# Optimization experiments

Measured on AMD Instinct MI355X. Metric: run time of the kernel, lower is better.

The kernel has to match this reference:

```python
import jax, jax.numpy as jnp
import numpy as np

T, D, H, E, K = 8192, 2048, 7168, 8, 2


def setup_inputs() -> dict:
    key = jax.random.key(0)
    ks = jax.random.split(key, 5)
    s = 0.02
    return {
        "x": jax.random.normal(ks[0], (T, D), jnp.float32),
        "gate_w": jax.random.normal(ks[1], (E, D), jnp.float32) * s,
        "w1": jax.random.normal(ks[2], (E, H, D), jnp.float32) * s,
        "w2": jax.random.normal(ks[3], (E, H, D), jnp.float32) * s,
        "w3": jax.random.normal(ks[4], (E, H, D), jnp.float32) * s,
    }


def reference(x, gate_w, w1, w2, w3):
    # gate logits [T, E]
    logits = x @ gate_w.T
    vals, idx = jax.lax.top_k(logits, K)                      # [T, K]
    w = jax.nn.softmax(vals.astype(jnp.float32), axis=-1).astype(x.dtype)
    # per-token routing weight for each expert (0 if not selected) [T, E]
    tok = jnp.arange(x.shape[0])
    expert_w = jnp.zeros((x.shape[0], E), x.dtype).at[tok[:, None], idx].add(w)

    # scan over experts: dense SwiGLU per expert, weighted accumulate
    def body(acc, ws):
        w1e, w2e, w3e, we = ws  # [H,D],[H,D],[H,D],[T]
        y = (jax.nn.silu(x @ w1e.T) * (x @ w3e.T)) @ w2e      # [T, D]
        return acc + we[:, None] * y, None

    res, _ = jax.lax.scan(body, jnp.zeros_like(x), (w1, w2, w3, expert_w.T))
    return res
```

## Files before the change

### kernel.cpp

```cpp
#include <hip/hip_runtime.h>

#define TT   8192
#define DDIM 2048
#define HDIM 7168
#define NEXP 8
#define MT   32
#define NT1  (HDIM / 128)
#define NT2  (DDIM / 256)
#define KSPL 2
#define NTILE_MAX 72

typedef __attribute__((ext_vector_type(8))) short bf16x8;
typedef __attribute__((ext_vector_type(8))) short short8v;
typedef __attribute__((ext_vector_type(4))) short short4v;
typedef __attribute__((ext_vector_type(4))) float f32x4;

__device__ __forceinline__ unsigned short f2bf(float f) {
  unsigned int u = __builtin_bit_cast(unsigned int, f);
  u += 0x7fffu + ((u >> 16) & 1u);
  return (unsigned short)(u >> 16);
}

__device__ __forceinline__ float bf2f(unsigned short h) {
  unsigned int u = ((unsigned int)h) << 16;
  return __builtin_bit_cast(float, u);
}

__device__ __forceinline__ void gload_lds16(const void* gp, void* lp) {
  __builtin_amdgcn_global_load_lds((__attribute__((address_space(1))) void*)gp,
                                   (__attribute__((address_space(3))) void*)lp,
                                   16, 0, 0);
}

__device__ __forceinline__ void mfma16(f32x4& c, bf16x8 a, bf16x8 b) {
  c = __builtin_amdgcn_mfma_f32_16x16x32_bf16(a, b, c, 0, 0, 0);
}

__device__ __forceinline__ void wg_barrier() {
  asm volatile("" ::: "memory");
  __builtin_amdgcn_s_barrier();
  asm volatile("" ::: "memory");
}

#define PH(H, BA, BB, RDB, STG, SRCP, SOFF, VM)                              \
  do {                                                                       \
    if (RDB) {                                                               \
      _Pragma("unroll")                                                      \
      for (int n = 0; n < 4; ++n)                                            \
        bfr[n] = *(const bf16x8*)(smem + (BB) + rB + n * 1024);              \
    }                                                                        \
    _Pragma("unroll")                                                        \
    for (int m = 0; m < 4; ++m)                                              \
      af[m] = *(const bf16x8*)(smem + (BA) + rA + ((H) + m) * 1024);         \
    if ((STG) >= 0) {                                                        \
      gload_lds16(SRCP[0] + (SOFF), smem + (STG) + wid * 2048);              \
      gload_lds16(SRCP[1] + (SOFF), smem + (STG) + wid * 2048 + 1024);       \
    }                                                                        \
    wg_barrier();                                                            \
    __builtin_amdgcn_s_setprio(1);                                           \
    _Pragma("unroll")                                                        \
    for (int n = 0; n < 4; ++n) {                                            \
      _Pragma("unroll")                                                      \
      for (int m = 0; m < 4; ++m)                                            \
        mfma16(acc[(H) + m][n], af[m], bfr[n]);                              \
    }                                                                        \
    __builtin_amdgcn_s_setprio(0);                                           \
    if ((VM) == 6) asm volatile("s_waitcnt vmcnt(6)" ::: "memory");          \
    if ((VM) == 0) asm volatile("s_waitcnt vmcnt(0)" ::: "memory");          \
    wg_barrier();                                                            \
  } while (0)

#define ITER_FULL(kb)                                                        \
  PH(0, 0,     32768,  1, 81920,  asrc, (kb) + 192, -1);                     \
  PH(4, 0,     32768,  0, 32768,  bsrc, (kb) + 256, -1);                     \
  PH(0, 16384, 49152,  1, 0,      asrc, (kb) + 256, -1);                     \
  PH(4, 16384, 49152,  0, 49152,  bsrc, (kb) + 320,  6);                     \
  PH(0, 65536, 98304,  1, 16384,  asrc, (kb) + 320, -1);                     \
  PH(4, 65536, 98304,  0, 98304,  bsrc, (kb) + 384, -1);                     \
  PH(0, 81920, 114688, 1, 65536,  asrc, (kb) + 384, -1);                     \
  PH(4, 81920, 114688, 0, 114688, bsrc, (kb) + 448,  6);

#define ITER_LAST(kb)                                                        \
  PH(0, 0,     32768,  1, 81920,  asrc, (kb) + 192, -1);                     \
  PH(4, 0,     32768,  0, -1,     asrc, 0,          -1);                     \
  PH(0, 16384, 49152,  1, -1,     asrc, 0,          -1);                     \
  PH(4, 16384, 49152,  0, -1,     asrc, 0,           0);                     \
  PH(0, 65536, 98304,  1, -1,     asrc, 0,          -1);                     \
  PH(4, 65536, 98304,  0, -1,     asrc, 0,          -1);                     \
  PH(0, 81920, 114688, 1, -1,     asrc, 0,          -1);                     \
  PH(4, 81920, 114688, 0, -1,     asrc, 0,          -1);

#define PROLOGUE()                                                           \
  do {                                                                       \
    gload_lds16(asrc[0] + 0,   smem + 0      + wid * 2048);                  \
    gload_lds16(asrc[1] + 0,   smem + 0      + wid * 2048 + 1024);           \
    gload_lds16(bsrc[0] + 0,   smem + 32768  + wid * 2048);                  \
    gload_lds16(bsrc[1] + 0,   smem + 32768  + wid * 2048 + 1024);           \
    gload_lds16(asrc[0] + 64,  smem + 16384  + wid * 2048);                  \
    gload_lds16(asrc[1] + 64,  smem + 16384  + wid * 2048 + 1024);           \
    gload_lds16(bsrc[0] + 64,  smem + 49152  + wid * 2048);                  \
    gload_lds16(bsrc[1] + 64,  smem + 49152  + wid * 2048 + 1024);           \
    gload_lds16(bsrc[0] + 128, smem + 98304  + wid * 2048);                  \
    gload_lds16(bsrc[1] + 128, smem + 98304  + wid * 2048 + 1024);           \
    gload_lds16(asrc[0] + 128, smem + 65536  + wid * 2048);                  \
    gload_lds16(asrc[1] + 128, smem + 65536  + wid * 2048 + 1024);           \
    gload_lds16(bsrc[0] + 192, smem + 114688 + wid * 2048);                  \
    gload_lds16(bsrc[1] + 192, smem + 114688 + wid * 2048 + 1024);           \
    asm volatile("s_waitcnt vmcnt(6)" ::: "memory");                         \
    wg_barrier();                                                            \
  } while (0)

__global__ __launch_bounds__(256) void cvt_bf16_kernel(const float* __restrict__ src,
                                                       unsigned short* __restrict__ dst,
                                                       long n8) {
  long i = (long)blockIdx.x * 256 + threadIdx.x;
  long stride = (long)gridDim.x * 256;
  for (; i < n8; i += stride) {
    float4 a = ((const float4*)src)[i * 2];
    float4 b = ((const float4*)src)[i * 2 + 1];
    short8v s;
    s[0] = (short)f2bf(a.x); s[1] = (short)f2bf(a.y);
    s[2] = (short)f2bf(a.z); s[3] = (short)f2bf(a.w);
    s[4] = (short)f2bf(b.x); s[5] = (short)f2bf(b.y);
    s[6] = (short)f2bf(b.z); s[7] = (short)f2bf(b.w);
    ((short8v*)dst)[i] = s;
  }
}

__global__ __launch_bounds__(256) void gate_kernel(const float* __restrict__ x,
                                                   const float* __restrict__ gw,
                                                   int* __restrict__ route_e,
                                                   float* __restrict__ route_w,
                                                   int* __restrict__ counts) {
  int t = blockIdx.x;
  int tid = threadIdx.x;
  const float* xr = x + (size_t)t * DDIM;
  float p[NEXP];
#pragma unroll
  for (int e = 0; e < NEXP; ++e) p[e] = 0.f;
#pragma unroll
  for (int c = 0; c < DDIM / (256 * 4); ++c) {
    int d = (c * 256 + tid) * 4;
    float4 xv = *(const float4*)(xr + d);
#pragma unroll
    for (int e = 0; e < NEXP; ++e) {
      float4 wv = *(const float4*)(gw + (size_t)e * DDIM + d);
      p[e] += xv.x * wv.x + xv.y * wv.y + xv.z * wv.z + xv.w * wv.w;
    }
  }
  __shared__ float red[NEXP][4];
  int lane = tid & 63, wid = tid >> 6;
#pragma unroll
  for (int e = 0; e < NEXP; ++e) {
    float v = p[e];
    for (int o = 32; o > 0; o >>= 1) v += __shfl_down(v, o);
    if (lane == 0) red[e][wid] = v;
  }
  __syncthreads();
  if (tid == 0) {
    float lg[NEXP];
#pragma unroll
    for (int e = 0; e < NEXP; ++e) lg[e] = red[e][0] + red[e][1] + red[e][2] + red[e][3];
    int i0 = 0;
#pragma unroll
    for (int e = 1; e < NEXP; ++e) if (lg[e] > lg[i0]) i0 = e;
    int i1 = -1;
#pragma unroll
    for (int e = 0; e < NEXP; ++e) {
      if (e == i0) continue;
      if (i1 < 0 || lg[e] > lg[i1]) i1 = e;
    }
    float w0 = 1.f / (1.f + __expf(lg[i1] - lg[i0]));
    float w1 = 1.f - w0;
    route_e[t * 2 + 0] = i0;  route_e[t * 2 + 1] = i1;
    route_w[t * 2 + 0] = w0;  route_w[t * 2 + 1] = w1;
    atomicAdd(&counts[i0], 1);
    atomicAdd(&counts[i1], 1);
  }
}

__global__ void scan_kernel(const int* __restrict__ counts, int* __restrict__ offsets,
                            int* __restrict__ cursor, int* __restrict__ tmap) {
  if (threadIdx.x == 0 && blockIdx.x == 0) {
    int o = 0, idx = 0;
    for (int e = 0; e < NEXP; ++e) {
      offsets[e] = o; cursor[e] = o;
      int c = counts[e]; o += c;
      for (int t = 0; t * 256 < c && idx < NTILE_MAX; ++t) tmap[1 + idx++] = (e << 16) | t;
    }
    tmap[0] = idx;
  }
}

__global__ __launch_bounds__(256) void scatter_kernel(const int* __restrict__ route_e,
                                                      const float* __restrict__ route_w,
                                                      int* __restrict__ cursor,
                                                      int* __restrict__ tok_list,
                                                      float* __restrict__ tok_w,
                                                      int* __restrict__ slot_of) {
  int t = blockIdx.x * 256 + threadIdx.x;
  if (t >= TT) return;
#pragma unroll
  for (int s = 0; s < 2; ++s) {
    int e = route_e[t * 2 + s];
    int p = atomicAdd(&cursor[e], 1);
    tok_list[p] = t;
    tok_w[p] = route_w[t * 2 + s];
    slot_of[t * 2 + s] = p;
  }
}

__global__ __launch_bounds__(256) void transpose_w2_kernel(const float* __restrict__ w2,
                                                           unsigned short* __restrict__ w2t,
                                                           int expert_fixed) {
  int e = expert_fixed >= 0 ? expert_fixed : (int)blockIdx.z;
  const float* src = w2 + (size_t)e * HDIM * DDIM;
  unsigned short* dst = w2t + (expert_fixed >= 0 ? (size_t)0 : (size_t)e * DDIM * HDIM);
  int h0 = blockIdx.x * 64, d0 = blockIdx.y * 64;
  __shared__ __align__(8) unsigned short tile[64 * 66];
  int tid = threadIdx.x;
  int hr = tid >> 2;
#pragma unroll
  for (int j = 0; j < 4; ++j) {
    int f4 = (tid & 3) + j * 4;
    float4 v = *(const float4*)(src + (size_t)(h0 + hr) * DDIM + d0 + f4 * 4);
    unsigned int lo = (unsigned int)f2bf(v.x) | ((unsigned int)f2bf(v.y) << 16);
    unsigned int hi = (unsigned int)f2bf(v.z) | ((unsigned int)f2bf(v.w) << 16);
    char* bp = (char*)tile + hr * 132 + f4 * 8;
    *(unsigned int*)bp = lo;
    *(unsigned int*)(bp + 4) = hi;
  }
  __syncthreads();
  int dr = tid >> 2;
  int hbase = (tid & 3) * 16;
  unsigned short vals[16];
#pragma unroll
  for (int i = 0; i < 16; ++i)
    vals[i] = *(unsigned short*)((char*)tile + (hbase + i) * 132 + dr * 2);
  unsigned short* op = dst + (size_t)(d0 + dr) * HDIM + h0 + hbase;
  short8v s0, s1;
#pragma unroll
  for (int i = 0; i < 8; ++i) { s0[i] = (short)vals[i]; s1[i] = (short)vals[i + 8]; }
  *(short8v*)(op) = s0;
  *(short8v*)(op + 8) = s1;
}

__global__ __launch_bounds__(256) void reduce_kernel(const unsigned short* __restrict__ ybuf,
                                                     const int* __restrict__ slot_of,
                                                     const float* __restrict__ route_w,
                                                     float* __restrict__ out) {
  const size_t YSZ = (size_t)TT * 2 * DDIM;
  int t = blockIdx.x;
  int d = threadIdx.x * 8;
  int s0 = slot_of[t * 2 + 0], s1 = slot_of[t * 2 + 1];
  float w0 = route_w[t * 2 + 0], w1 = route_w[t * 2 + 1];
  bf16x8 y0a = *(const bf16x8*)(ybuf + (size_t)s0 * DDIM + d);
  bf16x8 y0b = *(const bf16x8*)(ybuf + YSZ + (size_t)s0 * DDIM + d);
  bf16x8 y1a = *(const bf16x8*)(ybuf + (size_t)s1 * DDIM + d);
  bf16x8 y1b = *(const bf16x8*)(ybuf + YSZ + (size_t)s1 * DDIM + d);
  float* op = out + (size_t)t * DDIM + d;
#pragma unroll
  for (int j = 0; j < 8; ++j) {
    float v0 = bf2f((unsigned short)y0a[j]) + bf2f((unsigned short)y0b[j]);
    float v1 = bf2f((unsigned short)y1a[j]) + bf2f((unsigned short)y1b[j]);
    op[j] = w0 * v0 + w1 * v1;
  }
}

__global__ __launch_bounds__(512, 2) void gemm1_kernel(
    const unsigned short* __restrict__ xbf, const unsigned short* __restrict__ w1b,
    const unsigned short* __restrict__ w3b, const int* __restrict__ tok_list,
    const int* __restrict__ counts, const int* __restrict__ offsets,
    const int* __restrict__ tmap,
    unsigned short* __restrict__ g, int expert_fixed) {
  __shared__ __align__(16) char smem[133120];
  constexpr int NI = DDIM / 128;

  int nwg = gridDim.x;
  int orig = blockIdx.x;
  int wg = (orig & 7) * (nwg >> 3) + (orig >> 3);
  int e, mbase, nt;
  if (expert_fixed >= 0) {
    e = expert_fixed;
    mbase = (wg & (MT - 1)) * 256;
    nt = (wg >> 5) % NT1;
  } else {
    int tl = wg % NTILE_MAX;
    nt = wg / NTILE_MAX;
    if (tl >= tmap[0]) return;
    int pk = tmap[1 + tl];
    e = pk >> 16;
    mbase = (pk & 0xffff) * 256;
  }
  int cnt = counts[e];
  if (mbase >= cnt) return;
  int off = offsets[e];
  int gshift = expert_fixed >= 0 ? 0 : off;
  int rows = cnt - mbase; if (rows > 256) rows = 256;

  const unsigned short* w1e = expert_fixed >= 0 ? w1b : w1b + (size_t)e * HDIM * DDIM;
  const unsigned short* w3e = expert_fixed >= 0 ? w3b : w3b + (size_t)e * HDIM * DDIM;

  int tid = threadIdx.x, lane = tid & 63, wid = tid >> 6;
  int wr = wid >> 2, wc = wid & 3;

  int r16 = lane >> 2;
  int csrc = (lane & 3) ^ ((lane >> 3) & 3);
  const char* asrc[2]; const char* bsrc[2];
#pragma unroll
  for (int j = 0; j < 2; ++j) {
    int r = wid * 32 + j * 16 + r16;
    int m = mbase + r; if (m > cnt - 1) m = cnt - 1;
    int tok = tok_list[off + m];
    asrc[j] = (const char*)xbf + (size_t)tok * (DDIM * 2) + csrc * 16;
    const char* base = (r < 128)
        ? (const char*)w1e + (size_t)(nt * 128 + r) * (DDIM * 2)
        : (const char*)w3e + (size_t)(nt * 128 + r - 128) * (DDIM * 2);
    bsrc[j] = base + csrc * 16;
  }
  int rA = (wr * 128 + (lane & 15)) * 64 + (((lane >> 4) ^ ((lane >> 1) & 3)) * 16);
  int rB = (wc * 64  + (lane & 15)) * 64 + (((lane >> 4) ^ ((lane >> 1) & 3)) * 16);

  f32x4 zv = {0.f, 0.f, 0.f, 0.f};
  f32x4 acc[8][4];
#pragma unroll
  for (int m = 0; m < 8; ++m)
#pragma unroll
    for (int n = 0; n < 4; ++n) acc[m][n] = zv;
  bf16x8 af[4], bfr[4];

  PROLOGUE();
#pragma unroll 1
  for (int i = 0; i < NI - 1; ++i) {
    size_t kb = (size_t)i * 256;
    ITER_FULL(kb);
  }
  {
    size_t kb = (size_t)(NI - 1) * 256;
    ITER_LAST(kb);
  }

  float* hb = (float*)smem;
  if (wc < 2) {
#pragma unroll
    for (int m = 0; m < 8; ++m)
#pragma unroll
      for (int q = 0; q < 4; ++q) {
        int row = wr * 128 + m * 16 + (lane >> 4) * 4 + q;
        int col = wc * 64 + (lane & 15);
#pragma unroll
        for (int n = 0; n < 4; ++n)
          hb[row * 130 + col + n * 16] = acc[m][n][q];
      }
  }
  asm volatile("s_waitcnt lgkmcnt(0)" ::: "memory");
  wg_barrier();
  if (wc >= 2) {
#pragma unroll
    for (int m = 0; m < 8; ++m)
#pragma unroll
      for (int q = 0; q < 4; ++q) {
        int row = wr * 128 + m * 16 + (lane >> 4) * 4 + q;
        if (row >= rows) continue;
        size_t grow = (size_t)(mbase + row + gshift);
        int colbase = (wc - 2) * 64 + (lane & 15);
        unsigned short* gp = g + grow * HDIM + nt * 128 + colbase;
#pragma unroll
        for (int n = 0; n < 4; ++n) {
          float h1 = hb[row * 130 + colbase + n * 16];
          float h3 = acc[m][n][q];
          float gv = (h1 / (1.f + __expf(-h1))) * h3;
          gp[n * 16] = f2bf(gv);
        }
      }
  }
}

__global__ __launch_bounds__(512, 2) void gemm2_kernel(
    const unsigned short* __restrict__ g, const unsigned short* __restrict__ w2t,
    const int* __restrict__ tok_list, const float* __restrict__ tok_w,
    const int* __restrict__ counts, const int* __restrict__ offsets,
    const int* __restrict__ tmap,
    unsigned short* __restrict__ ybuf, float* __restrict__ out, int expert_fixed) {
  __shared__ __align__(16) char smem[131072];
  constexpr int NI = HDIM / 128 / KSPL;

  int nwg = gridDim.x;
  int orig = blockIdx.x;
  int wg = (orig & 7) * (nwg >> 3) + (orig >> 3);
  int e, mbase, nt, ks;
  if (expert_fixed >= 0) {
    e = expert_fixed;
    nt = wg % NT2;
    ks = (wg / NT2) % KSPL;
    mbase = (wg / (NT2 * KSPL)) * 256;
  } else {
    nt = wg % NT2;
    ks = (wg / NT2) % KSPL;
    int tl = wg / (NT2 * KSPL);
    if (tl >= tmap[0]) return;
    int pk = tmap[1 + tl];
    e = pk >> 16;
    mbase = (pk & 0xffff) * 256;
  }
  int cnt = counts[e];
  if (mbase >= cnt) return;
  int off = offsets[e];
  int gshift = expert_fixed >= 0 ? 0 : off;
  int nbase = nt * 256;
  int rows = cnt - mbase; if (rows > 256) rows = 256;
  const unsigned short* w2te = w2t + (expert_fixed >= 0 ? (size_t)0 : (size_t)e * DDIM * HDIM);
  size_t koff = (size_t)ks * (NI * 256);

  int tid = threadIdx.x, lane = tid & 63, wid = tid >> 6;
  int wr = wid >> 2, wc = wid & 3;

  int r16 = lane >> 2;
  int csrc = (lane & 3) ^ ((lane >> 3) & 3);
  const char* asrc[2]; const char* bsrc[2];
#pragma unroll
  for (int j = 0; j < 2; ++j) {
    int r = wid * 32 + j * 16 + r16;
    int m = mbase + r; if (m > cnt - 1) m = cnt - 1;
    asrc[j] = (const char*)g + (size_t)(m + gshift) * (HDIM * 2) + csrc * 16 + koff;
    bsrc[j] = (const char*)w2te + (size_t)(nbase + r) * (HDIM * 2) + csrc * 16 + koff;
  }
  int rA = (wr * 128 + (lane & 15)) * 64 + (((lane >> 4) ^ ((lane >> 1) & 3)) * 16);
  int rB = (wc * 64  + (lane & 15)) * 64 + (((lane >> 4) ^ ((lane >> 1) & 3)) * 16);

  f32x4 zv = {0.f, 0.f, 0.f, 0.f};
  f32x4 acc[8][4];
#pragma unroll
  for (int m = 0; m < 8; ++m)
#pragma unroll
    for (int n = 0; n < 4; ++n) acc[m][n] = zv;
  bf16x8 af[4], bfr[4];

  PROLOGUE();
#pragma unroll 1
  for (int i = 0; i < NI - 1; ++i) {
    size_t kb = (size_t)i * 256;
    ITER_FULL(kb);
  }
  {
    size_t kb = (size_t)(NI - 1) * 256;
    ITER_LAST(kb);
  }

  if (ybuf) {
    unsigned short* yb = ybuf + (size_t)ks * ((size_t)TT * 2 * DDIM);
#pragma unroll
    for (int m = 0; m < 8; ++m)
#pragma unroll
      for (int q = 0; q < 4; ++q) {
        int row = wr * 128 + m * 16 + (lane >> 4) * 4 + q;
        if (row >= rows) continue;
        size_t slot = (size_t)(off + mbase + row);
        unsigned short* yp = yb + slot * DDIM + nbase + wc * 64 + (lane & 15);
#pragma unroll
        for (int n = 0; n < 4; ++n)
          yp[n * 16] = f2bf(acc[m][n][q]);
      }
  } else {
#pragma unroll
    for (int m = 0; m < 8; ++m)
#pragma unroll
      for (int q = 0; q < 4; ++q) {
        int row = wr * 128 + m * 16 + (lane >> 4) * 4 + q;
        if (row >= rows) continue;
        int mi = mbase + row;
        int tok = tok_list[off + mi];
        float wt = tok_w[off + mi];
        float* op = out + (size_t)tok * DDIM + nbase + wc * 64 + (lane & 15);
#pragma unroll
        for (int n = 0; n < 4; ++n)
          atomicAdd(op + n * 16, acc[m][n][q] * wt);
      }
  }
}

extern "C" void kernel_launch(void* const* d_in, const int* in_sizes, int n_in,
                              void* d_out, int out_size, void* d_ws, size_t ws_size,
                              hipStream_t stream) {
  const float* x      = (const float*)d_in[0];
  const float* gate_w = (const float*)d_in[1];
  const float* w1     = (const float*)d_in[2];
  const float* w2     = (const float*)d_in[3];
  const float* w3     = (const float*)d_in[4];
  float* out = (float*)d_out;
  char* ws = (char*)d_ws;

  size_t o = 0;
  int* counts  = (int*)(ws + o);
  int* offsets = counts + 8;
  int* cursor  = counts + 16;
  int* tmap    = counts + 24;
  o += 1024;
  int*   route_e = (int*)(ws + o);   o += (size_t)TT * 2 * 4;
  float* route_w = (float*)(ws + o); o += (size_t)TT * 2 * 4;
  int*   tok_list = (int*)(ws + o);  o += (size_t)TT * 2 * 4;
  float* tok_w = (float*)(ws + o);   o += (size_t)TT * 2 * 4;
  int*   slot_of = (int*)(ws + o);   o += (size_t)TT * 2 * 4;
  unsigned short* xbf = (unsigned short*)(ws + o); o += (size_t)TT * DDIM * 2;
  size_t fixed = o;

  const size_t WSZ = (size_t)HDIM * DDIM;
  const size_t wbf_full = (size_t)NEXP * WSZ * 2;
  const size_t gfull = (size_t)TT * 2 * HDIM * 2;

  hipMemsetAsync(counts, 0, 8 * sizeof(int), stream);
  cvt_bf16_kernel<<<4096, 256, 0, stream>>>(x, xbf, (long)TT * DDIM / 8);
  gate_kernel<<<TT, 256, 0, stream>>>(x, gate_w, route_e, route_w, counts);
  scan_kernel<<<1, 64, 0, stream>>>(counts, offsets, cursor, tmap);
  scatter_kernel<<<(TT + 255) / 256, 256, 0, stream>>>(route_e, route_w, cursor,
                                                       tok_list, tok_w, slot_of);

  if (ws_size >= fixed + 3 * wbf_full + gfull) {
    unsigned short* w1b = (unsigned short*)(ws + fixed);
    unsigned short* w3b = w1b + NEXP * WSZ;
    unsigned short* w2t = w3b + NEXP * WSZ;
    unsigned short* gbuf = w2t + NEXP * WSZ;
    unsigned short* ybuf = w1b;
    cvt_bf16_kernel<<<8192, 256, 0, stream>>>(w1, w1b, (long)(NEXP * WSZ / 8));
    cvt_bf16_kernel<<<8192, 256, 0, stream>>>(w3, w3b, (long)(NEXP * WSZ / 8));
    transpose_w2_kernel<<<dim3(HDIM / 64, DDIM / 64, NEXP), 256, 0, stream>>>(w2, w2t, -1);
    gemm1_kernel<<<NTILE_MAX * NT1, 512, 0, stream>>>(
        xbf, w1b, w3b, tok_list, counts, offsets, tmap, gbuf, -1);
    gemm2_kernel<<<NTILE_MAX * NT2 * KSPL, 512, 0, stream>>>(
        gbuf, w2t, tok_list, tok_w, counts, offsets, tmap, ybuf, out, -1);
    reduce_kernel<<<TT, 256, 0, stream>>>(ybuf, slot_of, route_w, out);
  } else {
    unsigned short* w1b = (unsigned short*)(ws + fixed);
    unsigned short* w3b = w1b + WSZ;
    unsigned short* w2t = w3b + WSZ;
    unsigned short* gbuf = w2t + WSZ;
    hipMemsetAsync(out, 0, (size_t)TT * DDIM * sizeof(float), stream);
    for (int e = 0; e < NEXP; ++e) {
      cvt_bf16_kernel<<<4096, 256, 0, stream>>>(w1 + (size_t)e * WSZ, w1b, (long)(WSZ / 8));
      cvt_bf16_kernel<<<4096, 256, 0, stream>>>(w3 + (size_t)e * WSZ, w3b, (long)(WSZ / 8));
      transpose_w2_kernel<<<dim3(HDIM / 64, DDIM / 64, 1), 256, 0, stream>>>(w2, w2t, e);
      gemm1_kernel<<<MT * NT1, 512, 0, stream>>>(
          xbf, w1b, w3b, tok_list, counts, offsets, tmap, gbuf, e);
      gemm2_kernel<<<MT * NT2 * KSPL, 512, 0, stream>>>(
          gbuf, w2t, tok_list, tok_w, counts, offsets, tmap, (unsigned short*)0, out, e);
    }
  }
}
```

Baseline: 2.230 ms.

## Fuse x bf16 conversion into gate kernel and raise gemm2 split-K to four

The gate kernel now writes the bf16 copy of x while it reads x for the routing logits, so the separate conversion kernel and its second read of x are removed. Separately, the split-K factor for the second GEMM goes from 2 to 4, and the reduce kernel is generalised to sum KSPL partial buffers. The extra split gives gemm2 more workgroups to fill the GPU, at the cost of more bf16 partial traffic and precision loss in the reduce. The ybuf region (aliased onto w1b) must be large enough to hold four partial slices.

```diff
diff --git a/kernel.cpp b/kernel.cpp
--- a/kernel.cpp
+++ b/kernel.cpp
@@ -7,7 +7,7 @@
 #define MT   32
 #define NT1  (HDIM / 128)
 #define NT2  (DDIM / 256)
-#define KSPL 2
+#define KSPL 4
 #define NTILE_MAX 72
 
 typedef __attribute__((ext_vector_type(8))) short bf16x8;
@@ -131,10 +131,12 @@
                                                    const float* __restrict__ gw,
                                                    int* __restrict__ route_e,
                                                    float* __restrict__ route_w,
-                                                   int* __restrict__ counts) {
+                                                   int* __restrict__ counts,
+                                                   unsigned short* __restrict__ xbf) {
   int t = blockIdx.x;
   int tid = threadIdx.x;
   const float* xr = x + (size_t)t * DDIM;
+  unsigned short* xo = xbf + (size_t)t * DDIM;
   float p[NEXP];
 #pragma unroll
   for (int e = 0; e < NEXP; ++e) p[e] = 0.f;
@@ -142,6 +144,10 @@
   for (int c = 0; c < DDIM / (256 * 4); ++c) {
     int d = (c * 256 + tid) * 4;
     float4 xv = *(const float4*)(xr + d);
+    short4v s;
+    s[0] = (short)f2bf(xv.x); s[1] = (short)f2bf(xv.y);
+    s[2] = (short)f2bf(xv.z); s[3] = (short)f2bf(xv.w);
+    *(short4v*)(xo + d) = s;
 #pragma unroll
     for (int e = 0; e < NEXP; ++e) {
       float4 wv = *(const float4*)(gw + (size_t)e * DDIM + d);
@@ -254,17 +260,23 @@
   int d = threadIdx.x * 8;
   int s0 = slot_of[t * 2 + 0], s1 = slot_of[t * 2 + 1];
   float w0 = route_w[t * 2 + 0], w1 = route_w[t * 2 + 1];
-  bf16x8 y0a = *(const bf16x8*)(ybuf + (size_t)s0 * DDIM + d);
-  bf16x8 y0b = *(const bf16x8*)(ybuf + YSZ + (size_t)s0 * DDIM + d);
-  bf16x8 y1a = *(const bf16x8*)(ybuf + (size_t)s1 * DDIM + d);
-  bf16x8 y1b = *(const bf16x8*)(ybuf + YSZ + (size_t)s1 * DDIM + d);
+  float v0[8], v1[8];
+#pragma unroll
+  for (int j = 0; j < 8; ++j) { v0[j] = 0.f; v1[j] = 0.f; }
+#pragma unroll
+  for (int ks = 0; ks < KSPL; ++ks) {
+    bf16x8 y0 = *(const bf16x8*)(ybuf + (size_t)ks * YSZ + (size_t)s0 * DDIM + d);
+    bf16x8 y1 = *(const bf16x8*)(ybuf + (size_t)ks * YSZ + (size_t)s1 * DDIM + d);
+#pragma unroll
+    for (int j = 0; j < 8; ++j) {
+      v0[j] += bf2f((unsigned short)y0[j]);
+      v1[j] += bf2f((unsigned short)y1[j]);
+    }
+  }
   float* op = out + (size_t)t * DDIM + d;
 #pragma unroll
-  for (int j = 0; j < 8; ++j) {
-    float v0 = bf2f((unsigned short)y0a[j]) + bf2f((unsigned short)y0b[j]);
-    float v1 = bf2f((unsigned short)y1a[j]) + bf2f((unsigned short)y1b[j]);
-    op[j] = w0 * v0 + w1 * v1;
-  }
+  for (int j = 0; j < 8; ++j)
+    op[j] = w0 * v0[j] + w1 * v1[j];
 }
 
 __global__ __launch_bounds__(512, 2) void gemm1_kernel(
@@ -509,8 +521,7 @@
   const size_t gfull = (size_t)TT * 2 * HDIM * 2;
 
   hipMemsetAsync(counts, 0, 8 * sizeof(int), stream);
-  cvt_bf16_kernel<<<4096, 256, 0, stream>>>(x, xbf, (long)TT * DDIM / 8);
-  gate_kernel<<<TT, 256, 0, stream>>>(x, gate_w, route_e, route_w, counts);
+  gate_kernel<<<TT, 256, 0, stream>>>(x, gate_w, route_e, route_w, counts, xbf);
   scan_kernel<<<1, 64, 0, stream>>>(counts, offsets, cursor, tmap);
   scatter_kernel<<<(TT + 255) / 256, 256, 0, stream>>>(route_e, route_w, cursor,
                                                        tok_list, tok_w, slot_of);
```

Result: no change. 2.263 ms (+1.4%).
